# Kernel optimization log

Hardware: AMD Instinct MI355X
Metric: run time of the kernel (lower is better)

Reference implementation:

```python
import jax, jax.numpy as jnp
import numpy as np

N, C = 32768, 1000

def setup_inputs() -> dict:
    key = jax.random.key(0)
    k1, k2, k3 = jax.random.split(key, 3)
    out = jax.random.normal(k1, (N, C), dtype=jnp.float32)
    T = jax.random.uniform(k2, (C, C), dtype=jnp.float32)
    target = jax.random.randint(k3, (N,), 0, C, dtype=jnp.int64)
    return {"out": out, "T": T, "target": target}

def reference(out, T, target):
    # out: [N, C] logits, T: [C, C] transition matrix, target: [N] int labels
    n = out.shape[0]
    rows = jnp.arange(n)
    log_sm = jax.nn.log_softmax(out, axis=1)          # [N, C]
    sm = jnp.exp(log_sm)                              # softmax(out)
    pro1 = sm[rows, target]                           # softmax[i, y_i]
    # out_T[i] = T^T @ sm[i]  ->  out_T = sm @ T ; pro2 = out_T[i, y_i]
    pro2 = (sm @ T)[rows, target]
    # beta is detached in the original (Variable(...) breaks the graph)
    beta = jax.lax.stop_gradient(pro1 / pro2)         # [N]
    ce = -log_sm[rows, target]                        # per-sample cross entropy
    loss = jnp.sum(beta * ce) / n
    return loss
```

## Files before the change

### kernel.cpp

```cpp
#include <hip/hip_runtime.h>
#include <hip/hip_bf16.h>
#include <float.h>

#define RL_N 32768
#define RL_C 1000
#define TILE 32

__global__ __launch_bounds__(256) void transpose_kernel(
    const float* __restrict__ in, float* __restrict__ outp, int n) {
  __shared__ float tile[TILE][TILE + 1];
  int x = blockIdx.x * TILE + threadIdx.x;
  int y = blockIdx.y * TILE + threadIdx.y;
#pragma unroll
  for (int k = 0; k < TILE; k += 8) {
    int yy = y + k;
    if (x < n && yy < n) tile[threadIdx.y + k][threadIdx.x] = in[(size_t)yy * n + x];
  }
  __syncthreads();
  x = blockIdx.y * TILE + threadIdx.x;
  y = blockIdx.x * TILE + threadIdx.y;
#pragma unroll
  for (int k = 0; k < TILE; k += 8) {
    int yy = y + k;
    if (x < n && yy < n) outp[(size_t)yy * n + x] = tile[threadIdx.x][threadIdx.y + k];
  }
}

__device__ inline float wred_max(float v) {
#pragma unroll
  for (int o = 32; o > 0; o >>= 1) v = fmaxf(v, __shfl_down(v, o, 64));
  return v;
}
__device__ inline float wred_sum(float v) {
#pragma unroll
  for (int o = 32; o > 0; o >>= 1) v += __shfl_down(v, o, 64);
  return v;
}

__global__ __launch_bounds__(256) void row_kernel(
    const float* __restrict__ logits, const float* __restrict__ Tt,
    const int* __restrict__ target, float* __restrict__ partial) {
  const int row  = blockIdx.x;
  const int tid  = threadIdx.x;
  const int lane = tid & 63;
  const int wid  = tid >> 6;

  const int y = target[row];

  const float4* o4 = (const float4*)(logits + (size_t)row * RL_C);
  const float4* t4 = (const float4*)(Tt + (size_t)y * RL_C);

  const bool active = (tid < RL_C / 4);
  float4 ov = make_float4(0.f, 0.f, 0.f, 0.f);
  float4 tv = make_float4(0.f, 0.f, 0.f, 0.f);
  float lmax = -FLT_MAX;
  if (active) {
    ov = o4[tid];
    tv = t4[tid];
    lmax = fmaxf(fmaxf(ov.x, ov.y), fmaxf(ov.z, ov.w));
  }

  __shared__ float sm_m[4], sm_a[4], sm_b[4];

  float wm = wred_max(lmax);
  if (lane == 0) sm_m[wid] = wm;
  __syncthreads();
  const float m = fmaxf(fmaxf(sm_m[0], sm_m[1]), fmaxf(sm_m[2], sm_m[3]));

  float s1 = 0.f, s2 = 0.f;
  if (active) {
    float e0 = __expf(ov.x - m);
    float e1 = __expf(ov.y - m);
    float e2 = __expf(ov.z - m);
    float e3 = __expf(ov.w - m);
    s1 = (e0 + e1) + (e2 + e3);
    s2 = (e0 * tv.x + e1 * tv.y) + (e2 * tv.z + e3 * tv.w);
  }
  float ws1 = wred_sum(s1);
  float ws2 = wred_sum(s2);
  if (lane == 0) { sm_a[wid] = ws1; sm_b[wid] = ws2; }
  __syncthreads();

  if (tid == 0) {
    float s1t = (sm_a[0] + sm_a[1]) + (sm_a[2] + sm_a[3]);
    float s2t = (sm_b[0] + sm_b[1]) + (sm_b[2] + sm_b[3]);
    float oy  = logits[(size_t)row * RL_C + y];
    float beta = __expf(oy - m) / s2t;
    float ce   = (m + __logf(s1t)) - oy;
    partial[row] = beta * ce;
  }
}

__global__ __launch_bounds__(256) void reduce_kernel(
    const float* __restrict__ partial, float* __restrict__ outp, int n, float inv_n) {
  const int tid  = threadIdx.x;
  const int lane = tid & 63;
  const int wid  = tid >> 6;
  float s = 0.f;
  for (int i = tid; i < n; i += 256) s += partial[i];
  float ws = wred_sum(s);
  __shared__ float sm[4];
  if (lane == 0) sm[wid] = ws;
  __syncthreads();
  if (tid == 0) outp[0] = ((sm[0] + sm[1]) + (sm[2] + sm[3])) * inv_n;
}

extern "C" void kernel_launch(void* const* d_in, const int* in_sizes, int n_in,
                              void* d_out, int out_size, void* d_ws, size_t ws_size,
                              hipStream_t stream) {
  const float* logits = (const float*)d_in[0];
  const float* T      = (const float*)d_in[1];
  const int*   target = (const int*)d_in[2];
  float* outp = (float*)d_out;

  float* Tt      = (float*)d_ws;
  float* partial = (float*)((char*)d_ws + (size_t)RL_C * RL_C * sizeof(float));

  dim3 tb(TILE, 8);
  dim3 tg((RL_C + TILE - 1) / TILE, (RL_C + TILE - 1) / TILE);
  transpose_kernel<<<tg, tb, 0, stream>>>(T, Tt, RL_C);

  row_kernel<<<RL_N, 256, 0, stream>>>(logits, Tt, target, partial);

  reduce_kernel<<<1, 256, 0, stream>>>(partial, outp, RL_N, 1.0f / (float)RL_N);
}
```

Before: 223.9 us.

## Process each row with one wavefront and several rows per wave

Each row is now handled by a single 64-lane wavefront that loads four float4 chunks per lane, so the max and both sums come from wave shuffles (xor butterfly for the max) instead of block-wide shared-memory reductions with two __syncthreads. Each wave processes four rows and the per-block partials are pre-summed, so the launch shrinks from 32768 blocks to 2048 and the final reduce reads 2048 values. This targets launch and barrier overhead and the idle lanes of the old 256-thread-per-row layout, at the cost of more registers per thread and fewer blocks to hide memory latency.

```diff
diff --git a/kernel.cpp b/kernel.cpp
--- a/kernel.cpp
+++ b/kernel.cpp
@@ -4,7 +4,13 @@
 
 #define RL_N 32768
 #define RL_C 1000
+#define NVEC 250
 #define TILE 32
+
+#define ROW_BLOCKS 2048
+#define WAVES_PER_BLOCK 4
+#define TOTAL_WAVES (ROW_BLOCKS * WAVES_PER_BLOCK)
+#define ROWS_PER_WAVE (RL_N / TOTAL_WAVES)
 
 __global__ __launch_bounds__(256) void transpose_kernel(
     const float* __restrict__ in, float* __restrict__ outp, int n) {
@@ -26,12 +32,12 @@
   }
 }
 
-__device__ inline float wred_max(float v) {
+__device__ inline float wredmax_all(float v) {
 #pragma unroll
-  for (int o = 32; o > 0; o >>= 1) v = fmaxf(v, __shfl_down(v, o, 64));
+  for (int o = 32; o > 0; o >>= 1) v = fmaxf(v, __shfl_xor(v, o, 64));
   return v;
 }
-__device__ inline float wred_sum(float v) {
+__device__ inline float wredsum_l0(float v) {
 #pragma unroll
   for (int o = 32; o > 0; o >>= 1) v += __shfl_down(v, o, 64);
   return v;
@@ -40,65 +46,78 @@
 __global__ __launch_bounds__(256) void row_kernel(
     const float* __restrict__ logits, const float* __restrict__ Tt,
     const int* __restrict__ target, float* __restrict__ partial) {
-  const int row  = blockIdx.x;
   const int tid  = threadIdx.x;
   const int lane = tid & 63;
   const int wid  = tid >> 6;
+  const int wave = blockIdx.x * WAVES_PER_BLOCK + wid;
 
-  const int y = target[row];
+  const bool tail = lane < (NVEC - 192);
+  float acc = 0.f;
 
-  const float4* o4 = (const float4*)(logits + (size_t)row * RL_C);
-  const float4* t4 = (const float4*)(Tt + (size_t)y * RL_C);
+  const int row0 = wave * ROWS_PER_WAVE;
+#pragma unroll
+  for (int r = 0; r < ROWS_PER_WAVE; ++r) {
+    const int row = row0 + r;
+    const int y   = target[row];
 
-  const bool active = (tid < RL_C / 4);
-  float4 ov = make_float4(0.f, 0.f, 0.f, 0.f);
-  float4 tv = make_float4(0.f, 0.f, 0.f, 0.f);
-  float lmax = -FLT_MAX;
-  if (active) {
-    ov = o4[tid];
-    tv = t4[tid];
-    lmax = fmaxf(fmaxf(ov.x, ov.y), fmaxf(ov.z, ov.w));
+    const float4* o4 = (const float4*)(logits + (size_t)row * RL_C);
+    const float4* t4 = (const float4*)(Tt + (size_t)y * RL_C);
+
+    float4 ov0 = o4[lane], ov1 = o4[lane + 64], ov2 = o4[lane + 128];
+    float4 tv0 = t4[lane], tv1 = t4[lane + 64], tv2 = t4[lane + 128];
+    float4 ov3 = make_float4(-FLT_MAX, -FLT_MAX, -FLT_MAX, -FLT_MAX);
+    float4 tv3 = make_float4(0.f, 0.f, 0.f, 0.f);
+    if (tail) { ov3 = o4[lane + 192]; tv3 = t4[lane + 192]; }
+
+    float lm = fmaxf(fmaxf(fmaxf(ov0.x, ov0.y), fmaxf(ov0.z, ov0.w)),
+                     fmaxf(fmaxf(ov1.x, ov1.y), fmaxf(ov1.z, ov1.w)));
+    lm = fmaxf(lm, fmaxf(fmaxf(ov2.x, ov2.y), fmaxf(ov2.z, ov2.w)));
+    lm = fmaxf(lm, fmaxf(fmaxf(ov3.x, ov3.y), fmaxf(ov3.z, ov3.w)));
+    const float m = wredmax_all(lm);
+
+    float e0x = __expf(ov0.x - m), e0y = __expf(ov0.y - m),
+          e0z = __expf(ov0.z - m), e0w = __expf(ov0.w - m);
+    float e1x = __expf(ov1.x - m), e1y = __expf(ov1.y - m),
+          e1z = __expf(ov1.z - m), e1w = __expf(ov1.w - m);
+    float e2x = __expf(ov2.x - m), e2y = __expf(ov2.y - m),
+          e2z = __expf(ov2.z - m), e2w = __expf(ov2.w - m);
+    float e3x = __expf(ov3.x - m), e3y = __expf(ov3.y - m),
+          e3z = __expf(ov3.z - m), e3w = __expf(ov3.w - m);
+
+    float s1 = ((e0x + e0y) + (e0z + e0w)) + ((e1x + e1y) + (e1z + e1w))
+             + ((e2x + e2y) + (e2z + e2w)) + ((e3x + e3y) + (e3z + e3w));
+    float s2 = ((e0x * tv0.x + e0y * tv0.y) + (e0z * tv0.z + e0w * tv0.w))
+             + ((e1x * tv1.x + e1y * tv1.y) + (e1z * tv1.z + e1w * tv1.w))
+             + ((e2x * tv2.x + e2y * tv2.y) + (e2z * tv2.z + e2w * tv2.w))
+             + ((e3x * tv3.x + e3y * tv3.y) + (e3z * tv3.z + e3w * tv3.w));
+
+    float s1t = wredsum_l0(s1);
+    float s2t = wredsum_l0(s2);
+
+    if (lane == 0) {
+      const float oy = logits[(size_t)row * RL_C + y];
+      const float beta = __expf(oy - m) / s2t;
+      const float ce   = (m + __logf(s1t)) - oy;
+      acc += beta * ce;
+    }
   }
 
-  __shared__ float sm_m[4], sm_a[4], sm_b[4];
-
-  float wm = wred_max(lmax);
-  if (lane == 0) sm_m[wid] = wm;
+  __shared__ float sm[WAVES_PER_BLOCK];
+  if (lane == 0) sm[wid] = acc;
   __syncthreads();
-  const float m = fmaxf(fmaxf(sm_m[0], sm_m[1]), fmaxf(sm_m[2], sm_m[3]));
-
-  float s1 = 0.f, s2 = 0.f;
-  if (active) {
-    float e0 = __expf(ov.x - m);
-    float e1 = __expf(ov.y - m);
-    float e2 = __expf(ov.z - m);
-    float e3 = __expf(ov.w - m);
-    s1 = (e0 + e1) + (e2 + e3);
-    s2 = (e0 * tv.x + e1 * tv.y) + (e2 * tv.z + e3 * tv.w);
-  }
-  float ws1 = wred_sum(s1);
-  float ws2 = wred_sum(s2);
-  if (lane == 0) { sm_a[wid] = ws1; sm_b[wid] = ws2; }
-  __syncthreads();
-
-  if (tid == 0) {
-    float s1t = (sm_a[0] + sm_a[1]) + (sm_a[2] + sm_a[3]);
-    float s2t = (sm_b[0] + sm_b[1]) + (sm_b[2] + sm_b[3]);
-    float oy  = logits[(size_t)row * RL_C + y];
-    float beta = __expf(oy - m) / s2t;
-    float ce   = (m + __logf(s1t)) - oy;
-    partial[row] = beta * ce;
-  }
+  if (tid == 0)
+    partial[blockIdx.x] = (sm[0] + sm[1]) + (sm[2] + sm[3]);
 }
 
 __global__ __launch_bounds__(256) void reduce_kernel(
-    const float* __restrict__ partial, float* __restrict__ outp, int n, float inv_n) {
+    const float* __restrict__ partial, float* __restrict__ outp, float inv_n) {
   const int tid  = threadIdx.x;
   const int lane = tid & 63;
   const int wid  = tid >> 6;
   float s = 0.f;
-  for (int i = tid; i < n; i += 256) s += partial[i];
-  float ws = wred_sum(s);
+#pragma unroll
+  for (int i = tid; i < ROW_BLOCKS; i += 256) s += partial[i];
+  float ws = wredsum_l0(s);
   __shared__ float sm[4];
   if (lane == 0) sm[wid] = ws;
   __syncthreads();
@@ -120,7 +139,7 @@
   dim3 tg((RL_C + TILE - 1) / TILE, (RL_C + TILE - 1) / TILE);
   transpose_kernel<<<tg, tb, 0, stream>>>(T, Tt, RL_C);
 
-  row_kernel<<<RL_N, 256, 0, stream>>>(logits, Tt, target, partial);
+  row_kernel<<<ROW_BLOCKS, 256, 0, stream>>>(logits, Tt, target, partial);
 
-  reduce_kernel<<<1, 256, 0, stream>>>(partial, outp, RL_N, 1.0f / (float)RL_N);
+  reduce_kernel<<<1, 256, 0, stream>>>(partial, outp, 1.0f / (float)RL_N);
 }
```

Measured after the change: 197.4 us. -11.8%, faster.
